# Kernel optimization log

Hardware: AMD Instinct MI355X
Metric: run time of the kernel (lower is better)

Reference implementation:

```python
import jax, jax.numpy as jnp
import numpy as np

B, S, H, I, G = 4, 2048, 2048, 8192, 128


def _onebit_quant(w, group_size):
    # Group-wise 1-bit (sign) quantization along the input dim with per-group
    # abs-mean scale, as in BitNet-style OneBitLinear.
    out_f, in_f = w.shape
    wg = w.reshape(out_f, in_f // group_size, group_size)
    scale = jnp.mean(jnp.abs(wg), axis=-1, keepdims=True)  # [out, n_groups, 1]
    wq = jnp.sign(wg) * scale
    return wq.reshape(out_f, in_f)


def setup_inputs() -> dict:
    key = jax.random.key(0)
    k1, k2, k3, k4 = jax.random.split(key, 4)
    return {
        "x": jax.random.normal(k1, (B, S, H), dtype=jnp.float32),
        "w_gate": jax.random.normal(k2, (I, H), dtype=jnp.float32) * 0.02,
        "w_up": jax.random.normal(k3, (I, H), dtype=jnp.float32) * 0.02,
        "w_down": jax.random.normal(k4, (H, I), dtype=jnp.float32) * 0.02,
        "group_size": G,
    }


def reference(x, w_gate, w_up, w_down, group_size):
    wg_q = _onebit_quant(w_gate, group_size)   # [I, H]
    wu_q = _onebit_quant(w_up, group_size)     # [I, H]
    wd_q = _onebit_quant(w_down, group_size)   # [H, I]
    gate = jnp.einsum('bsh,ih->bsi', x, wg_q)  # [B, S, I]
    up = jnp.einsum('bsh,ih->bsi', x, wu_q)    # [B, S, I]
    h = jax.nn.silu(gate) * up                 # [B, S, I]
    return jnp.einsum('bsi,hi->bsh', h, wd_q)  # [B, S, H]
```

## Files before the change

### kernel.cpp

```cpp
#include <hip/hip_runtime.h>
#include <hip/hip_bf16.h>
#include <cstdint>
#include <cstddef>

using bf16 = __hip_bfloat16;

typedef __attribute__((ext_vector_type(8))) short short8;
typedef __attribute__((ext_vector_type(4))) float f32x4;
typedef __attribute__((ext_vector_type(4))) unsigned short us4;

static constexpr int Bb = 4, Ss = 2048, Hh = 2048, Ii = 8192, Gg = 128;
static constexpr int Mm = Bb * Ss;

#define MEMFENCE() asm volatile("" ::: "memory")
#define BARRIER() do { MEMFENCE(); __builtin_amdgcn_s_barrier(); MEMFENCE(); } while (0)

__global__ void quant_onebit(const float* __restrict__ w, bf16* __restrict__ wq,
                             int ngroups) {
  int gid = blockIdx.x * 4 + (threadIdx.x >> 6);
  if (gid >= ngroups) return;
  int lane = threadIdx.x & 63;
  size_t base = (size_t)gid * Gg + (size_t)lane * 2;
  float2 v = *(const float2*)(w + base);
  float s = fabsf(v.x) + fabsf(v.y);
#pragma unroll
  for (int m = 32; m >= 1; m >>= 1) s += __shfl_xor(s, m);
  float scale = s * (1.0f / 128.0f);
  float q0 = (v.x > 0.f) ? scale : ((v.x < 0.f) ? -scale : 0.f);
  float q1 = (v.y > 0.f) ? scale : ((v.y < 0.f) ? -scale : 0.f);
  unsigned int p =
      (unsigned int)__builtin_bit_cast(unsigned short, __float2bfloat16(q0)) |
      ((unsigned int)__builtin_bit_cast(unsigned short, __float2bfloat16(q1)) << 16);
  *(unsigned int*)(wq + base) = p;
}

__global__ void cast_f32_bf16(const float* __restrict__ in, bf16* __restrict__ out,
                              size_t n4) {
  size_t i = (size_t)blockIdx.x * blockDim.x + threadIdx.x;
  if (i >= n4) return;
  float4 v = *(const float4*)(in + i * 4);
  us4 o;
  o.x = __builtin_bit_cast(unsigned short, __float2bfloat16(v.x));
  o.y = __builtin_bit_cast(unsigned short, __float2bfloat16(v.y));
  o.z = __builtin_bit_cast(unsigned short, __float2bfloat16(v.z));
  o.w = __builtin_bit_cast(unsigned short, __float2bfloat16(v.w));
  *(us4*)(out + i * 4) = o;
}

__device__ __forceinline__ void gload16(const bf16* g, char* l) {
  __builtin_amdgcn_global_load_lds(
      (const __attribute__((address_space(1))) void*)g,
      (__attribute__((address_space(3))) void*)l, 16, 0, 0);
}

__device__ __forceinline__ short8 lfrag(const char* part, int row, int s) {
  return *(const short8*)(part + row * 64 + (((s ^ (row >> 1)) & 3) << 4));
}

template <bool DUAL>
__global__ __launch_bounds__(512, 2)
void gemm_bt8(const bf16* __restrict__ A,
              const bf16* __restrict__ B0,
              const bf16* __restrict__ B1,
              bf16* __restrict__ OutBf,
              float* __restrict__ OutF,
              int M, int N, int K) {
  constexpr int BM = 256, BN = DUAL ? 128 : 256;
  constexpr int NF = DUAL ? 2 : 4;
  extern __shared__ char smem[];

  const int tid = threadIdx.x;
  const int wid = tid >> 6;
  const int lane = tid & 63;
  const int wr = wid >> 2;
  const int wc = wid & 3;
  const int lrow = lane & 15;
  const int ks = lane >> 4;

  const int nbx = N / BN;
  const int nbm = M / BM;
  const int nwg = (int)gridDim.x;
  const int cpx = nwg >> 3;
  const int wg = (int)blockIdx.x;
  const int L = (wg & 7) * cpx + (wg >> 3);
  constexpr int CN = 8;
  const int chunk = L / (nbm * CN);
  const int within = L % (nbm * CN);
  const int m0 = (within / CN) * BM;
  const int n0 = (chunk * CN + (within % CN)) * BN;

  const int NT = K / 64;

  const int srow = tid >> 2;
  const int slog8 = (((tid & 3) ^ ((tid >> 3) & 3)) << 3);
  const bf16* pA0 = A + (size_t)(m0 + srow) * K + slog8;
  const bf16* pA1 = pA0 + (size_t)128 * K;
  const bf16* pB0 = B0 + (size_t)(n0 + srow) * K + slog8;
  const bf16* pB1 = DUAL ? (B1 + (size_t)(n0 + srow) * K + slog8)
                         : (pB0 + (size_t)128 * K);
  const int dA = wid * 1024;

  auto stageA = [&](int t, int p) {
    char* b = smem + (size_t)(t & 1) * 65536 + p * 32768;
    const int koff = t * 64 + p * 32;
    gload16(pA0 + koff, b + dA);
    gload16(pA1 + koff, b + 8192 + dA);
  };
  auto stageB = [&](int t, int p) {
    char* b = smem + (size_t)(t & 1) * 65536 + p * 32768 + 16384;
    const int koff = t * 64 + p * 32;
    gload16(pB0 + koff, b + dA);
    gload16(pB1 + koff, b + 8192 + dA);
  };

  const f32x4 vzero = {0.f, 0.f, 0.f, 0.f};
  f32x4 acc0[8][NF];
  f32x4 acc1[DUAL ? 8 : 1][NF];
#pragma unroll
  for (int mf = 0; mf < 8; ++mf)
#pragma unroll
    for (int nf = 0; nf < NF; ++nf) {
      acc0[mf][nf] = vzero;
      if constexpr (DUAL) acc1[mf][nf] = vzero;
    }

  stageA(0, 0); stageB(0, 0);
  stageA(0, 1); stageB(0, 1);

  short8 fa[4], fb0[NF], fb1[DUAL ? NF : 1];

  for (int t = 0; t < NT; ++t) {
    const char* buf = smem + (size_t)(t & 1) * 65536;
#pragma unroll
    for (int p = 0; p < 2; ++p) {
      const char* Ap = buf + p * 32768;
      const char* Bp = Ap + 16384;

      if (p == 0 || t + 1 < NT)
        asm volatile("s_waitcnt vmcnt(4)" ::: "memory");
      else
        asm volatile("s_waitcnt vmcnt(0)" ::: "memory");
      BARRIER();
      if constexpr (DUAL) {
#pragma unroll
        for (int nf = 0; nf < 2; ++nf) {
          fb0[nf] = lfrag(Bp, wc * 32 + nf * 16 + lrow, ks);
          fb1[nf] = lfrag(Bp + 8192, wc * 32 + nf * 16 + lrow, ks);
        }
      } else {
#pragma unroll
        for (int nf = 0; nf < 4; ++nf)
          fb0[nf] = lfrag(Bp, wc * 64 + nf * 16 + lrow, ks);
      }
#pragma unroll
      for (int i = 0; i < 4; ++i)
        fa[i] = lfrag(Ap, wr * 128 + i * 16 + lrow, ks);
      if (t + 1 < NT) stageA(t + 1, p);
      __builtin_amdgcn_s_setprio(1);
#pragma unroll
      for (int i = 0; i < 4; ++i)
#pragma unroll
        for (int nf = 0; nf < NF; ++nf) {
          acc0[i][nf] = __builtin_amdgcn_mfma_f32_16x16x32_bf16(
              fa[i], fb0[nf], acc0[i][nf], 0, 0, 0);
          if constexpr (DUAL)
            acc1[i][nf] = __builtin_amdgcn_mfma_f32_16x16x32_bf16(
                fa[i], fb1[nf], acc1[i][nf], 0, 0, 0);
        }
      __builtin_amdgcn_s_setprio(0);
      BARRIER();

#pragma unroll
      for (int i = 0; i < 4; ++i)
        fa[i] = lfrag(Ap, wr * 128 + 64 + i * 16 + lrow, ks);
      if (t + 1 < NT) stageB(t + 1, p);
      __builtin_amdgcn_s_setprio(1);
#pragma unroll
      for (int i = 0; i < 4; ++i)
#pragma unroll
        for (int nf = 0; nf < NF; ++nf) {
          acc0[4 + i][nf] = __builtin_amdgcn_mfma_f32_16x16x32_bf16(
              fa[i], fb0[nf], acc0[4 + i][nf], 0, 0, 0);
          if constexpr (DUAL)
            acc1[4 + i][nf] = __builtin_amdgcn_mfma_f32_16x16x32_bf16(
                fa[i], fb1[nf], acc1[4 + i][nf], 0, 0, 0);
        }
      __builtin_amdgcn_s_setprio(0);
    }
  }

  const int crow0 = (lane >> 4) * 4;
  const int ccol = lane & 15;
#pragma unroll
  for (int mf = 0; mf < 8; ++mf)
#pragma unroll
    for (int nf = 0; nf < NF; ++nf)
#pragma unroll
      for (int j = 0; j < 4; ++j) {
        const int row = m0 + wr * 128 + mf * 16 + crow0 + j;
        if constexpr (DUAL) {
          const int col = n0 + wc * 32 + nf * 16 + ccol;
          float g = acc0[mf][nf][j];
          float u = acc1[mf][nf][j];
          OutBf[(size_t)row * N + col] =
              __float2bfloat16(g / (1.0f + expf(-g)) * u);
        } else {
          const int col = n0 + wc * 64 + nf * 16 + ccol;
          OutF[(size_t)row * N + col] = acc0[mf][nf][j];
        }
      }
}

extern "C" void kernel_launch(void* const* d_in, const int* in_sizes, int n_in,
                              void* d_out, int out_size, void* d_ws, size_t ws_size,
                              hipStream_t stream) {
  const float* x = (const float*)d_in[0];
  const float* wg = (const float*)d_in[1];
  const float* wu = (const float*)d_in[2];
  const float* wd = (const float*)d_in[3];
  float* out = (float*)d_out;

  char* ws = (char*)d_ws;
  bf16* xq = (bf16*)(ws + 0);
  bf16* wgq = (bf16*)(ws + (size_t)33554432);
  bf16* wuq = (bf16*)(ws + (size_t)67108864);
  bf16* hbuf = (bf16*)(ws + (size_t)100663296);
  bf16* wdq = xq;

  auto* kDual = gemm_bt8<true>;
  auto* kSingle = gemm_bt8<false>;
  (void)hipFuncSetAttribute((const void*)kDual,
                            hipFuncAttributeMaxDynamicSharedMemorySize, 131072);
  (void)hipFuncSetAttribute((const void*)kSingle,
                            hipFuncAttributeMaxDynamicSharedMemorySize, 131072);

  const int ngW = (Ii * Hh) / Gg;
  quant_onebit<<<ngW / 4, 256, 0, stream>>>(wg, wgq, ngW);
  quant_onebit<<<ngW / 4, 256, 0, stream>>>(wu, wuq, ngW);

  const size_t n4 = (size_t)Mm * Hh / 4;
  cast_f32_bf16<<<(unsigned)((n4 + 255) / 256), 256, 0, stream>>>(x, xq, n4);

  kDual<<<(Mm / 256) * (Ii / 128), 512, 131072, stream>>>(
      xq, wgq, wuq, hbuf, nullptr, Mm, Ii, Hh);

  quant_onebit<<<ngW / 4, 256, 0, stream>>>(wd, wdq, ngW);

  kSingle<<<(Mm / 256) * (Hh / 256), 512, 131072, stream>>>(
      hbuf, wdq, nullptr, nullptr, out, Mm, Hh, Ii);
}
```

Baseline: 818.5 us.

## Switch GEMM kernels from 16x16x32 to 32x32x16 MFMA tiles

Replaces the 16x16x32 bf16 MFMA fragments with 32x32x16 MFMA instructions in both the dual gate/up GEMM and the down GEMM. This restructures the register fragment layout, LDS fragment loads and epilogue indexing. The goal is fewer instructions and fewer LDS fragment reads per unit of work, since each B fragment is reused across 32 rows. The trade-off is a changed accumulator layout and K-split ordering across the two half-phases, and the epilogue stores must map rows correctly.

Result: slower. 885.7 us (+8.2%).

```diff
diff --git a/kernel.cpp b/kernel.cpp
--- a/kernel.cpp
+++ b/kernel.cpp
@@ -6,7 +6,7 @@
 using bf16 = __hip_bfloat16;
 
 typedef __attribute__((ext_vector_type(8))) short short8;
-typedef __attribute__((ext_vector_type(4))) float f32x4;
+typedef __attribute__((ext_vector_type(16))) float f32x16;
 typedef __attribute__((ext_vector_type(4))) unsigned short us4;
 
 static constexpr int Bb = 4, Ss = 2048, Hh = 2048, Ii = 8192, Gg = 128;
@@ -66,7 +66,6 @@
               float* __restrict__ OutF,
               int M, int N, int K) {
   constexpr int BM = 256, BN = DUAL ? 128 : 256;
-  constexpr int NF = DUAL ? 2 : 4;
   extern __shared__ char smem[];
 
   const int tid = threadIdx.x;
@@ -74,8 +73,8 @@
   const int lane = tid & 63;
   const int wr = wid >> 2;
   const int wc = wid & 3;
-  const int lrow = lane & 15;
-  const int ks = lane >> 4;
+  const int l31 = lane & 31;
+  const int lh = lane >> 5;
 
   const int nbx = N / BN;
   const int nbm = M / BM;
@@ -113,21 +112,19 @@
     gload16(pB1 + koff, b + 8192 + dA);
   };
 
-  const f32x4 vzero = {0.f, 0.f, 0.f, 0.f};
-  f32x4 acc0[8][NF];
-  f32x4 acc1[DUAL ? 8 : 1][NF];
-#pragma unroll
-  for (int mf = 0; mf < 8; ++mf)
-#pragma unroll
-    for (int nf = 0; nf < NF; ++nf) {
-      acc0[mf][nf] = vzero;
-      if constexpr (DUAL) acc1[mf][nf] = vzero;
-    }
+  const int aRowBase = wr * 128 + l31;
+  const int bRow0 = (DUAL ? wc * 32 : wc * 64) + l31;
+  const int bRow1 = DUAL ? bRow0 : (bRow0 + 32);
+
+  const f32x16 vzero = {0.f};
+  f32x16 acc0[4], acc1[4];
+#pragma unroll
+  for (int mf = 0; mf < 4; ++mf) { acc0[mf] = vzero; acc1[mf] = vzero; }
 
   stageA(0, 0); stageB(0, 0);
   stageA(0, 1); stageB(0, 1);
 
-  short8 fa[4], fb0[NF], fb1[DUAL ? NF : 1];
+  short8 fa[4], fb0k[2], fb1k[2];
 
   for (int t = 0; t < NT; ++t) {
     const char* buf = smem + (size_t)(t & 1) * 65536;
@@ -135,80 +132,66 @@
     for (int p = 0; p < 2; ++p) {
       const char* Ap = buf + p * 32768;
       const char* Bp = Ap + 16384;
+      const char* Bp1 = DUAL ? (Bp + 8192) : Bp;
 
       if (p == 0 || t + 1 < NT)
         asm volatile("s_waitcnt vmcnt(4)" ::: "memory");
       else
         asm volatile("s_waitcnt vmcnt(0)" ::: "memory");
       BARRIER();
-      if constexpr (DUAL) {
-#pragma unroll
-        for (int nf = 0; nf < 2; ++nf) {
-          fb0[nf] = lfrag(Bp, wc * 32 + nf * 16 + lrow, ks);
-          fb1[nf] = lfrag(Bp + 8192, wc * 32 + nf * 16 + lrow, ks);
-        }
-      } else {
-#pragma unroll
-        for (int nf = 0; nf < 4; ++nf)
-          fb0[nf] = lfrag(Bp, wc * 64 + nf * 16 + lrow, ks);
-      }
-#pragma unroll
-      for (int i = 0; i < 4; ++i)
-        fa[i] = lfrag(Ap, wr * 128 + i * 16 + lrow, ks);
+#pragma unroll
+      for (int ku = 0; ku < 2; ++ku) {
+        fb0k[ku] = lfrag(Bp, bRow0, ku * 2 + lh);
+        fb1k[ku] = lfrag(Bp1, bRow1, ku * 2 + lh);
+      }
+#pragma unroll
+      for (int mf = 0; mf < 4; ++mf)
+        fa[mf] = lfrag(Ap, aRowBase + mf * 32, lh);
       if (t + 1 < NT) stageA(t + 1, p);
       __builtin_amdgcn_s_setprio(1);
 #pragma unroll
-      for (int i = 0; i < 4; ++i)
-#pragma unroll
-        for (int nf = 0; nf < NF; ++nf) {
-          acc0[i][nf] = __builtin_amdgcn_mfma_f32_16x16x32_bf16(
-              fa[i], fb0[nf], acc0[i][nf], 0, 0, 0);
-          if constexpr (DUAL)
-            acc1[i][nf] = __builtin_amdgcn_mfma_f32_16x16x32_bf16(
-                fa[i], fb1[nf], acc1[i][nf], 0, 0, 0);
-        }
+      for (int mf = 0; mf < 4; ++mf) {
+        acc0[mf] = __builtin_amdgcn_mfma_f32_32x32x16_bf16(
+            fa[mf], fb0k[0], acc0[mf], 0, 0, 0);
+        acc1[mf] = __builtin_amdgcn_mfma_f32_32x32x16_bf16(
+            fa[mf], fb1k[0], acc1[mf], 0, 0, 0);
+      }
       __builtin_amdgcn_s_setprio(0);
       BARRIER();
 
 #pragma unroll
-      for (int i = 0; i < 4; ++i)
-        fa[i] = lfrag(Ap, wr * 128 + 64 + i * 16 + lrow, ks);
+      for (int mf = 0; mf < 4; ++mf)
+        fa[mf] = lfrag(Ap, aRowBase + mf * 32, 2 + lh);
       if (t + 1 < NT) stageB(t + 1, p);
       __builtin_amdgcn_s_setprio(1);
 #pragma unroll
-      for (int i = 0; i < 4; ++i)
-#pragma unroll
-        for (int nf = 0; nf < NF; ++nf) {
-          acc0[4 + i][nf] = __builtin_amdgcn_mfma_f32_16x16x32_bf16(
-              fa[i], fb0[nf], acc0[4 + i][nf], 0, 0, 0);
-          if constexpr (DUAL)
-            acc1[4 + i][nf] = __builtin_amdgcn_mfma_f32_16x16x32_bf16(
-                fa[i], fb1[nf], acc1[4 + i][nf], 0, 0, 0);
-        }
+      for (int mf = 0; mf < 4; ++mf) {
+        acc0[mf] = __builtin_amdgcn_mfma_f32_32x32x16_bf16(
+            fa[mf], fb0k[1], acc0[mf], 0, 0, 0);
+        acc1[mf] = __builtin_amdgcn_mfma_f32_32x32x16_bf16(
+            fa[mf], fb1k[1], acc1[mf], 0, 0, 0);
+      }
       __builtin_amdgcn_s_setprio(0);
     }
   }
 
-  const int crow0 = (lane >> 4) * 4;
-  const int ccol = lane & 15;
-#pragma unroll
-  for (int mf = 0; mf < 8; ++mf)
-#pragma unroll
-    for (int nf = 0; nf < NF; ++nf)
-#pragma unroll
-      for (int j = 0; j < 4; ++j) {
-        const int row = m0 + wr * 128 + mf * 16 + crow0 + j;
-        if constexpr (DUAL) {
-          const int col = n0 + wc * 32 + nf * 16 + ccol;
-          float g = acc0[mf][nf][j];
-          float u = acc1[mf][nf][j];
-          OutBf[(size_t)row * N + col] =
-              __float2bfloat16(g / (1.0f + expf(-g)) * u);
-        } else {
-          const int col = n0 + wc * 64 + nf * 16 + ccol;
-          OutF[(size_t)row * N + col] = acc0[mf][nf][j];
-        }
-      }
+#pragma unroll
+  for (int mf = 0; mf < 4; ++mf)
+#pragma unroll
+    for (int r = 0; r < 16; ++r) {
+      const int row = m0 + wr * 128 + mf * 32 + (r & 3) + 8 * (r >> 2) + 4 * lh;
+      if constexpr (DUAL) {
+        const int col = n0 + wc * 32 + l31;
+        float g = acc0[mf][r];
+        float u = acc1[mf][r];
+        OutBf[(size_t)row * N + col] =
+            __float2bfloat16(g / (1.0f + expf(-g)) * u);
+      } else {
+        const int col = n0 + wc * 64 + l31;
+        OutF[(size_t)row * N + col] = acc0[mf][r];
+        OutF[(size_t)row * N + col + 32] = acc1[mf][r];
+      }
+    }
 }
 
 extern "C" void kernel_launch(void* const* d_in, const int* in_sizes, int n_in,
```

## Software-pipeline LDS fragment reads with MFMA and halve barriers per K-step

Applied to the files above, without the earlier changes.

Restructures the GEMM main loop so the A/B fragments for the next MFMA slot are read from LDS into a second register set while the current slot's MFMAs issue. This cuts the number of workgroup barriers per 64-wide K tile from four to two. The global-to-LDS staging is re-timed to match, with adjusted vmcnt waits. The aim is to hide LDS read latency and barrier stalls behind matrix work. The cost is more live fragment registers under the 2-waves-per-SIMD launch bound, and tighter buffer-reuse ordering that must stay race-free.

New measurement: 824.1 us. Within noise of the previous version (+0.7%).

```diff
diff --git a/kernel.cpp b/kernel.cpp
--- a/kernel.cpp
+++ b/kernel.cpp
@@ -113,6 +113,27 @@
     gload16(pB1 + koff, b + 8192 + dA);
   };
 
+  short8 fa_cur[4], fa_nxt[4];
+  short8 fbs0[4], fbs1[4];
+
+  auto readFA = [&](short8* dst, const char* Ap, int h) {
+#pragma unroll
+    for (int i = 0; i < 4; ++i)
+      dst[i] = lfrag(Ap, wr * 128 + h * 64 + i * 16 + lrow, ks);
+  };
+  auto readFB = [&](short8* dst, const char* Bp) {
+    if constexpr (DUAL) {
+      dst[0] = lfrag(Bp, wc * 32 + lrow, ks);
+      dst[1] = lfrag(Bp, wc * 32 + 16 + lrow, ks);
+      dst[2] = lfrag(Bp + 8192, wc * 32 + lrow, ks);
+      dst[3] = lfrag(Bp + 8192, wc * 32 + 16 + lrow, ks);
+    } else {
+#pragma unroll
+      for (int nf = 0; nf < 4; ++nf)
+        dst[nf] = lfrag(Bp, wc * 64 + nf * 16 + lrow, ks);
+    }
+  };
+
   const f32x4 vzero = {0.f, 0.f, 0.f, 0.f};
   f32x4 acc0[8][NF];
   f32x4 acc1[DUAL ? 8 : 1][NF];
@@ -124,69 +145,63 @@
       if constexpr (DUAL) acc1[mf][nf] = vzero;
     }
 
+  auto mfmaSlot = [&](int h, const short8* fa, const short8* fb) {
+#pragma unroll
+    for (int mf = 0; mf < 4; ++mf)
+#pragma unroll
+      for (int nf = 0; nf < NF; ++nf) {
+        acc0[h * 4 + mf][nf] = __builtin_amdgcn_mfma_f32_16x16x32_bf16(
+            fa[mf], fb[nf], acc0[h * 4 + mf][nf], 0, 0, 0);
+        if constexpr (DUAL)
+          acc1[h * 4 + mf][nf] = __builtin_amdgcn_mfma_f32_16x16x32_bf16(
+              fa[mf], fb[2 + nf], acc1[h * 4 + mf][nf], 0, 0, 0);
+      }
+  };
+
   stageA(0, 0); stageB(0, 0);
   stageA(0, 1); stageB(0, 1);
-
-  short8 fa[4], fb0[NF], fb1[DUAL ? NF : 1];
+  asm volatile("s_waitcnt vmcnt(4)" ::: "memory");
+  BARRIER();
+  readFA(fa_cur, smem, 0);
+  readFB(fbs0, smem + 16384);
 
   for (int t = 0; t < NT; ++t) {
-    const char* buf = smem + (size_t)(t & 1) * 65536;
-#pragma unroll
-    for (int p = 0; p < 2; ++p) {
-      const char* Ap = buf + p * 32768;
-      const char* Bp = Ap + 16384;
-
-      if (p == 0 || t + 1 < NT)
-        asm volatile("s_waitcnt vmcnt(4)" ::: "memory");
-      else
-        asm volatile("s_waitcnt vmcnt(0)" ::: "memory");
-      BARRIER();
-      if constexpr (DUAL) {
-#pragma unroll
-        for (int nf = 0; nf < 2; ++nf) {
-          fb0[nf] = lfrag(Bp, wc * 32 + nf * 16 + lrow, ks);
-          fb1[nf] = lfrag(Bp + 8192, wc * 32 + nf * 16 + lrow, ks);
-        }
-      } else {
-#pragma unroll
-        for (int nf = 0; nf < 4; ++nf)
-          fb0[nf] = lfrag(Bp, wc * 64 + nf * 16 + lrow, ks);
-      }
-#pragma unroll
-      for (int i = 0; i < 4; ++i)
-        fa[i] = lfrag(Ap, wr * 128 + i * 16 + lrow, ks);
-      if (t + 1 < NT) stageA(t + 1, p);
-      __builtin_amdgcn_s_setprio(1);
-#pragma unroll
-      for (int i = 0; i < 4; ++i)
-#pragma unroll
-        for (int nf = 0; nf < NF; ++nf) {
-          acc0[i][nf] = __builtin_amdgcn_mfma_f32_16x16x32_bf16(
-              fa[i], fb0[nf], acc0[i][nf], 0, 0, 0);
-          if constexpr (DUAL)
-            acc1[i][nf] = __builtin_amdgcn_mfma_f32_16x16x32_bf16(
-                fa[i], fb1[nf], acc1[i][nf], 0, 0, 0);
-        }
-      __builtin_amdgcn_s_setprio(0);
-      BARRIER();
-
-#pragma unroll
-      for (int i = 0; i < 4; ++i)
-        fa[i] = lfrag(Ap, wr * 128 + 64 + i * 16 + lrow, ks);
-      if (t + 1 < NT) stageB(t + 1, p);
-      __builtin_amdgcn_s_setprio(1);
-#pragma unroll
-      for (int i = 0; i < 4; ++i)
-#pragma unroll
-        for (int nf = 0; nf < NF; ++nf) {
-          acc0[4 + i][nf] = __builtin_amdgcn_mfma_f32_16x16x32_bf16(
-              fa[i], fb0[nf], acc0[4 + i][nf], 0, 0, 0);
-          if constexpr (DUAL)
-            acc1[4 + i][nf] = __builtin_amdgcn_mfma_f32_16x16x32_bf16(
-                fa[i], fb1[nf], acc1[4 + i][nf], 0, 0, 0);
-        }
-      __builtin_amdgcn_s_setprio(0);
+    const char* bufc = smem + (size_t)(t & 1) * 65536;
+    const char* bufn = smem + (size_t)((t + 1) & 1) * 65536;
+    const bool more = (t + 1 < NT);
+
+    readFA(fa_nxt, bufc, 1);
+    if (more) stageA(t + 1, 0);
+    __builtin_amdgcn_s_setprio(1);
+    mfmaSlot(0, fa_cur, fbs0);
+    __builtin_amdgcn_s_setprio(0);
+
+    if (more) asm volatile("s_waitcnt vmcnt(2)" ::: "memory");
+    else      asm volatile("s_waitcnt vmcnt(0)" ::: "memory");
+    BARRIER();
+    readFA(fa_cur, bufc + 32768, 0);
+    readFB(fbs1, bufc + 32768 + 16384);
+    if (more) stageB(t + 1, 0);
+    __builtin_amdgcn_s_setprio(1);
+    mfmaSlot(1, fa_nxt, fbs0);
+    __builtin_amdgcn_s_setprio(0);
+
+    readFA(fa_nxt, bufc + 32768, 1);
+    if (more) stageA(t + 1, 1);
+    __builtin_amdgcn_s_setprio(1);
+    mfmaSlot(0, fa_cur, fbs1);
+    __builtin_amdgcn_s_setprio(0);
+
+    asm volatile("s_waitcnt vmcnt(2)" ::: "memory");
+    BARRIER();
+    if (more) {
+      readFA(fa_cur, bufn, 0);
+      readFB(fbs0, bufn + 16384);
+      stageB(t + 1, 1);
     }
+    __builtin_amdgcn_s_setprio(1);
+    mfmaSlot(1, fa_nxt, fbs1);
+    __builtin_amdgcn_s_setprio(0);
   }
 
   const int crow0 = (lane >> 4) * 4;
```
